# Optimization experiments

Hardware: AMD Instinct MI355X
Metric: run time of the kernel (lower is better)

## Reference

```python
import jax, jax.numpy as jnp
import numpy as np
from jax import lax


def _conv(x, W):
    # NCHW conv, stride 1, SAME padding (padding = kernel//2 in original)
    return lax.conv_general_dilated(x, W, (1, 1), 'SAME',
                                    dimension_numbers=('NCHW', 'OIHW', 'NCHW'))


def _cconv(zr, zi, Wr, Wi, br, bi):
    # complex conv: (zr + i*zi) * (Wr + i*Wi)
    yr = _conv(zr, Wr) - _conv(zi, Wi) + br[None, :, None, None]
    yi = _conv(zr, Wi) + _conv(zi, Wr) + bi[None, :, None, None]
    return yr, yi


def setup_inputs() -> dict:
    key = jax.random.key(0)
    B, C, H, W = 16, 128, 64, 64        # C = 128 total = 64 real + 64 imag channels
    half = C // 2                        # 64 complex channels
    kin = (C + C) // 2                   # (input+hidden)/2 complex input channels = 128
    K = 3
    ks = jax.random.split(key, 20)
    inp = {
        'x':      jax.random.normal(ks[0], (B, C, H, W), jnp.float32),
        'h_prev': jax.random.normal(ks[1], (B, C, H, W), jnp.float32),
        'c_prev': jax.random.normal(ks[2], (B, C, H, W), jnp.float32),
    }
    i = 3
    for g in ('i', 'f', 'o', 'c'):
        inp['Wr_' + g] = jax.random.normal(ks[i], (half, kin, K, K), jnp.float32) * 0.05; i += 1
        inp['Wi_' + g] = jax.random.normal(ks[i], (half, kin, K, K), jnp.float32) * 0.05; i += 1
        inp['br_' + g] = jax.random.normal(ks[i], (half,), jnp.float32) * 0.05; i += 1
        inp['bi_' + g] = jax.random.normal(ks[i], (half,), jnp.float32) * 0.05; i += 1
    return inp


def reference(x, h_prev, c_prev,
              Wr_i, Wi_i, br_i, bi_i,
              Wr_f, Wi_f, br_f, bi_f,
              Wr_o, Wi_o, br_o, bi_o,
              Wr_c, Wi_c, br_c, bi_c):
    C = x.shape[1]
    h = C // 2
    xr, xi = x[:, :h], x[:, h:]
    hr, hi = h_prev[:, :h], h_prev[:, h:]
    cr, ci = c_prev[:, :h], c_prev[:, h:]

    zr = jnp.concatenate([xr, hr], axis=1)   # real part of combined
    zi = jnp.concatenate([xi, hi], axis=1)   # imag part of combined

    # gates: complex conv then split sigmoid / tanh (applied per component)
    i_r, i_i = map(jax.nn.sigmoid, _cconv(zr, zi, Wr_i, Wi_i, br_i, bi_i))
    # f gate conv output is computed but unused in final update (original bug keeps x as f)
    o_r, o_i = map(jax.nn.sigmoid, _cconv(zr, zi, Wr_o, Wi_o, br_o, bi_o))
    ct_r, ct_i = map(jnp.tanh, _cconv(zr, zi, Wr_c, Wi_c, br_c, bi_c))

    # faithful to original: f_r/f_i taken from x, not from conv_f output
    c_new_r = xr * cr - xi * ci + i_r * ct_r - i_i * ct_i
    c_new_i = xr * ci + xi * cr + i_r * ct_i + i_i * ct_r

    t_r = jnp.tanh(c_new_r)
    t_i = jnp.tanh(c_new_i)
    h_new = jnp.concatenate([o_r * t_r - o_i * t_i, o_r * t_i + o_i * t_r], axis=1)
    c_new = jnp.concatenate([c_new_r, c_new_i], axis=1)
    return h_new, c_new
```

## Files before the change

kernel.cpp:

```cpp
#include <hip/hip_runtime.h>
#include <hip/hip_bf16.h>


typedef __attribute__((ext_vector_type(8))) short short8;
typedef __attribute__((ext_vector_type(4))) float floatx4;
typedef __attribute__((ext_vector_type(4))) float float4v;

#define HSIZE  8388608

__device__ __forceinline__ short f2bf(float f) {
  __hip_bfloat16 h = __float2bfloat16(f);
  return *reinterpret_cast<short*>(&h);
}

__device__ __forceinline__ float bf2f(short s) {
  unsigned u = ((unsigned)(unsigned short)s) << 16;
  return __uint_as_float(u);
}

__device__ __forceinline__ void gload16(const short* g, void* lds) {
  __builtin_amdgcn_global_load_lds(
      (__attribute__((address_space(1))) void*)(g),
      (__attribute__((address_space(3))) void*)(lds), 16, 0, 0);
}

__global__ __launch_bounds__(256) void prep_kernel(
    const float* __restrict__ xs, const float* __restrict__ hs,
    short* __restrict__ Zp,
    const float* __restrict__ Wr_i, const float* __restrict__ Wi_i,
    const float* __restrict__ Wr_o, const float* __restrict__ Wi_o,
    const float* __restrict__ Wr_c, const float* __restrict__ Wi_c,
    const float* __restrict__ br_i, const float* __restrict__ bi_i,
    const float* __restrict__ br_o, const float* __restrict__ bi_o,
    const float* __restrict__ br_c, const float* __restrict__ bi_c,
    short* __restrict__ Wp, float* __restrict__ bias) {
  __shared__ short tile[64 * 72];
  int blk = blockIdx.x;
  int tid = threadIdx.x;

  if (blk < 520) {
    int t = blk * 256 + tid;
    int s   = t & 31;
    int pix = t >> 5;
    int b = pix / 260;
    int r = pix - b * 260;
    int yp, xp;
    if (r < 66)       { yp = 0;               xp = r; }
    else if (r < 132) { yp = 65;              xp = r - 66; }
    else { int r2 = r - 132; yp = 1 + (r2 >> 1); xp = (r2 & 1) * 65; }
    short8 z;
#pragma unroll
    for (int q = 0; q < 8; ++q) z[q] = 0;
    *(short8*)(Zp + (((b * 66 + yp) * 66 + xp) * 256 + s * 8)) = z;
    return;
  }

  if (blk < 520 + 4096) {
    int bid = blk - 520;
    int y      = bid & 63;
    int half   = (bid >> 6) & 1;
    int srcSel = (bid >> 7) & 1;
    int b      = bid >> 8;
    const float* src = srcSel ? hs : xs;
    int chBase  = half * 64;
    int cinBase = half * 128 + srcSel * 64;
    int x4 = tid & 15, chq = tid >> 4;
#pragma unroll
    for (int p = 0; p < 4; ++p) {
      int ch = p * 16 + chq;
      float4v f = *(const float4v*)(src + (size_t)(b * 128 + chBase + ch) * 4096 + y * 64 + x4 * 4);
#pragma unroll
      for (int e = 0; e < 4; ++e)
        tile[(x4 * 4 + e) * 72 + ch] = f2bf(f[e]);
    }
    __syncthreads();
    int x = tid >> 2, seg = tid & 3;
    short8 v0 = *(const short8*)(tile + x * 72 + seg * 16);
    short8 v1 = *(const short8*)(tile + x * 72 + seg * 16 + 8);
    size_t outp = ((size_t)(b * 66 + y + 1) * 66 + x + 1) * 256 + cinBase + seg * 16;
    *(short8*)(Zp + outp)     = v0;
    *(short8*)(Zp + outp + 8) = v1;
    return;
  }

  {
    int g = (blk - 4616) * 256 + tid;
    if (g >= 384 * 9 * 256) return;
    int cin = g & 255;
    int tap = (g >> 8) % 9;
    int n   = g / (256 * 9);
    int part = n >> 6, ch = n & 63;
    const float *Wr, *Wi;
    if (part < 2)      { Wr = Wr_i; Wi = Wi_i; }
    else if (part < 4) { Wr = Wr_o; Wi = Wi_o; }
    else               { Wr = Wr_c; Wi = Wi_c; }
    int im = part & 1;
    int ci = cin & 127;
    int second = cin >> 7;
    const float* src = im ? (second ? Wr : Wi) : (second ? Wi : Wr);
    float f = src[(ch * 128 + ci) * 9 + tap];
    if (!im && second) f = -f;
    Wp[(n * 9 + tap) * 256 + cin] = f2bf(f);
    if (g < 384) {
      int p2 = g >> 6, c2 = g & 63;
      const float* bs = (p2 == 0) ? br_i : (p2 == 1) ? bi_i : (p2 == 2) ? br_o
                      : (p2 == 3) ? bi_o : (p2 == 4) ? br_c : bi_c;
      bias[g] = bs[c2];
    }
  }
}

__device__ __forceinline__ void issueA(const short* __restrict__ Wp, int tapkc,
                                       short8* dst, int tid, int wv) {
#pragma unroll
  for (int it = 0; it < 3; ++it) {
    int idx = tid + it * 512;
    int row = idx >> 2, p = idx & 3;
    int g = p ^ (row & 3);
    gload16(Wp + ((size_t)row * 2304 + tapkc + g * 8),
            (void*)(dst + (it * 512 + wv * 64)));
  }
}

__device__ __forceinline__ void issueBc(const short* __restrict__ Z, int zrow0,
                                        int kcn32, int tapc, short8* dst,
                                        int tid, int wv) {
  int idx = tapc * 512 + tid;
  int row = idx >> 8;
  int rem = idx & 255;
  int col = 1 + (rem >> 2);
  int p   = idx & 3;
  int g   = p ^ (col & 3);
  int base = tapc * 512 + wv * 64;
  int rowu = base >> 8;
  gload16(Z + ((size_t)((zrow0 + row) * 66 + col) * 256 + kcn32 + g * 8),
          (void*)(dst + (base + rowu * 8 + 4)));
}

template<int DYN, int DXN>
__device__ __forceinline__ void readFrags(const short8* __restrict__ Ab,
                                          const short8* __restrict__ Bb0,
                                          short8 (&af)[6], short8 (&bf)[4],
                                          int aBase, int wpx, int l15, int l4) {
  const short8* Bb = Bb0 + (wpx + DYN) * 264;
  int bb = (l15 + DXN) * 4 + (l4 ^ ((l15 + DXN) & 3));
#pragma unroll
  for (int i = 0; i < 6; ++i) af[i] = Ab[aBase + i * 64];
#pragma unroll
  for (int j = 0; j < 4; ++j) bf[j] = Bb[bb + j * 64];
}

__device__ __forceinline__ void mfma24(const short8 (&af)[6], const short8 (&bf)[4],
                                       floatx4 (&acc)[6][4]) {
  __builtin_amdgcn_s_setprio(1);
#pragma unroll
  for (int i = 0; i < 6; ++i)
#pragma unroll
    for (int j = 0; j < 4; ++j)
      acc[i][j] = __builtin_amdgcn_mfma_f32_16x16x32_bf16(af[i], bf[j], acc[i][j], 0, 0, 0);
  __builtin_amdgcn_s_setprio(0);
}

__device__ __forceinline__ float fsig(float v) { return 1.f / (1.f + __expf(-v)); }
__device__ __forceinline__ float ftanh(float v) {
  float e = __expf(2.f * v);
  return 1.f - 2.f / (e + 1.f);
}

__global__ __launch_bounds__(512, 2) void conv_fused(
    const short* __restrict__ Z, const short* __restrict__ Wp,
    const float* __restrict__ bias, const float* __restrict__ x,
    const float* __restrict__ c_prev, float* __restrict__ out) {
  __shared__ short8 As[2][1536];
  __shared__ short8 Bs[2][1056];

  const int tid = threadIdx.x;
  const int wv = tid >> 6, lane = tid & 63;
  const int l15 = lane & 15, l4 = lane >> 4;
  const int wc4 = wv & 3;
  const int wpx = wv >> 2;
  const int pb = blockIdx.x;
  const int b  = pb >> 5;
  const int y0 = (pb & 31) * 2;
  const int zrow0 = b * 66 + y0;

  const int aBase = (wc4 * 96 + l15) * 4 + (l4 ^ (l15 & 3));

  floatx4 acc[6][4];
#pragma unroll
  for (int i = 0; i < 6; ++i)
#pragma unroll
    for (int j = 0; j < 4; ++j)
#pragma unroll
      for (int r = 0; r < 4; ++r) acc[i][j][r] = 0.f;

  short8 afA[6], bfA[4], afB[6], bfB[4];

  if (tid < 64) {
    int buf = tid >> 5, w = tid & 31;
    int r = w >> 3, hi = (w >> 2) & 1, p = w & 3;
    short8 z;
#pragma unroll
    for (int q = 0; q < 8; ++q) z[q] = 0;
    Bs[buf][r * 264 + (hi ? 260 : 0) + p] = z;
  }
  issueA(Wp, 0, &As[0][0], tid, wv);
  issueBc(Z, zrow0, 0, 0, &Bs[0][0], tid, wv);
  issueBc(Z, zrow0, 0, 1, &Bs[0][0], tid, wv);
  issueA(Wp, 256, &As[1][0], tid, wv);
  __builtin_amdgcn_sched_barrier(0);
  asm volatile("s_waitcnt vmcnt(3) lgkmcnt(0)" ::: "memory");
  __builtin_amdgcn_sched_barrier(0);
  __builtin_amdgcn_s_barrier();
  __builtin_amdgcn_sched_barrier(0);
  readFrags<0, 0>(&As[0][0], &Bs[0][0], afA, bfA, aBase, wpx, l15, l4);

#define STEP(TAP, PE, KCV)                                                     \
  {                                                                            \
    constexpr int PS   = ((TAP) + (PE)) & 1;                                   \
    constexpr int TAPN = ((TAP) + 1) % 9;                                      \
    constexpr int PBN  = ((TAP) == 8) ? ((PE) ^ 1) : (PE);                     \
    if constexpr ((TAP) == 1 || (TAP) == 2)                                    \
      asm volatile("s_waitcnt vmcnt(1) lgkmcnt(0)" ::: "memory");              \
    else                                                                       \
      asm volatile("s_waitcnt vmcnt(0) lgkmcnt(0)" ::: "memory");              \
    __builtin_amdgcn_sched_barrier(0);                                         \
    __builtin_amdgcn_s_barrier();                                              \
    __builtin_amdgcn_sched_barrier(0);                                         \
    if constexpr (PS == 0)                                                     \
      readFrags<TAPN / 3, TAPN % 3>(&As[1][0], &Bs[PBN][0], afB, bfB,          \
                                    aBase, wpx, l15, l4);                      \
    else                                                                       \
      readFrags<TAPN / 3, TAPN % 3>(&As[0][0], &Bs[PBN][0], afA, bfA,          \
                                    aBase, wpx, l15, l4);                      \
    { const int kc2 = ((TAP) <= 6) ? (KCV) : (KCV) + 1;                        \
      issueA(Wp, (((TAP) + 2) % 9) * 256 + kc2 * 32, &As[PS][0], tid, wv); }   \
    if constexpr ((TAP) == 0 || (TAP) == 1)                                    \
      issueBc(Z, zrow0, ((KCV) + 1) * 32, (TAP), &Bs[(PE) ^ 1][0], tid, wv);   \
    if constexpr (PS == 0) mfma24(afA, bfA, acc);                              \
    else                   mfma24(afB, bfB, acc);                              \
  }

  for (int kq = 0; kq < 4; ++kq) {
    const int kE = kq * 2, kO = kE + 1;
    STEP(0, 0, kE) STEP(1, 0, kE) STEP(2, 0, kE) STEP(3, 0, kE) STEP(4, 0, kE)
    STEP(5, 0, kE) STEP(6, 0, kE) STEP(7, 0, kE) STEP(8, 0, kE)
    STEP(0, 1, kO) STEP(1, 1, kO) STEP(2, 1, kO) STEP(3, 1, kO) STEP(4, 1, kO)
    STEP(5, 1, kO) STEP(6, 1, kO) STEP(7, 1, kO) STEP(8, 1, kO)
  }
#undef STEP

  asm volatile("s_waitcnt vmcnt(0) lgkmcnt(0)" ::: "memory");
  __syncthreads();
  short* Ex = (short*)&As[0][0];
#pragma unroll
  for (int l = 0; l < 2; ++l) {
    if (wpx == l) {
#pragma unroll
      for (int i = 0; i < 6; ++i)
#pragma unroll
        for (int j = 0; j < 4; ++j)
#pragma unroll
          for (int rr = 0; rr < 4; ++rr) {
            int ch = wc4 * 96 + i * 16 + l4 * 4 + rr;
            int xx = j * 16 + l15;
            Ex[ch * 64 + xx] = f2bf(acc[i][j][rr] + bias[ch]);
          }
    }
    __syncthreads();
    {
      int xg = tid & 63, cg = tid >> 6;
#pragma unroll
      for (int k = 0; k < 8; ++k) {
        int c = cg * 8 + k;
        float yri = bf2f(Ex[(0 * 64 + c) * 64 + xg]);
        float yii = bf2f(Ex[(1 * 64 + c) * 64 + xg]);
        float yro = bf2f(Ex[(2 * 64 + c) * 64 + xg]);
        float yio = bf2f(Ex[(3 * 64 + c) * 64 + xg]);
        float yrc = bf2f(Ex[(4 * 64 + c) * 64 + xg]);
        float yic = bf2f(Ex[(5 * 64 + c) * 64 + xg]);
        float i_r = fsig(yri), i_i = fsig(yii);
        float o_r = fsig(yro), o_i = fsig(yio);
        float ct_r = ftanh(yrc), ct_i = ftanh(yic);
        int base = (b * 128 + c) * 4096 + (y0 + l) * 64 + xg;
        float xr = x[base];
        float xi = x[base + 64 * 4096];
        float cr = c_prev[base];
        float ci = c_prev[base + 64 * 4096];
        float cnr = xr * cr - xi * ci + i_r * ct_r - i_i * ct_i;
        float cni = xr * ci + xi * cr + i_r * ct_i + i_i * ct_r;
        float tr = ftanh(cnr), ti = ftanh(cni);
        out[base]                     = o_r * tr - o_i * ti;
        out[base + 64 * 4096]         = o_r * ti + o_i * tr;
        out[HSIZE + base]             = cnr;
        out[HSIZE + base + 64 * 4096] = cni;
      }
    }
    __syncthreads();
  }
}

extern "C" void kernel_launch(void* const* d_in, const int* in_sizes, int n_in,
                              void* d_out, int out_size, void* d_ws, size_t ws_size,
                              hipStream_t stream) {
  char* ws = (char*)d_ws;
  short* Zp   = (short*)ws;
  short* Wp   = (short*)(ws + 35684352);
  float* bias = (float*)(ws + 37453824);

  prep_kernel<<<8072, 256, 0, stream>>>(
      (const float*)d_in[0], (const float*)d_in[1], Zp,
      (const float*)d_in[3], (const float*)d_in[4],
      (const float*)d_in[11], (const float*)d_in[12],
      (const float*)d_in[15], (const float*)d_in[16],
      (const float*)d_in[5], (const float*)d_in[6],
      (const float*)d_in[13], (const float*)d_in[14],
      (const float*)d_in[17], (const float*)d_in[18],
      Wp, bias);
  conv_fused<<<512, 512, 0, stream>>>(
      Zp, Wp, bias, (const float*)d_in[0], (const float*)d_in[2],
      (float*)d_out);
}
```

Baseline: 310.0 us.

## Rework LDS swizzles for A/B tiles, drop prep transpose tile, pad epilogue staging

Changes the global-to-LDS load mapping for weight and input tiles so each row pair shares an 8-slot swizzled group, and updates the fragment reads to match, aiming to cut LDS bank conflicts in the MFMA loop. The prep kernel's activation transpose now builds bf16 channel vectors directly in registers from float2 loads, with no shared-memory tile or barrier. The epilogue staging buffer is split into two channel halves with a padded row stride of 68, which lowers bank conflicts but adds an extra barrier round per output row.

New measurement: 314.8 us. No clear change (+1.6%).

```diff
diff --git a/kernel.cpp b/kernel.cpp
--- a/kernel.cpp
+++ b/kernel.cpp
@@ -5,6 +5,7 @@
 typedef __attribute__((ext_vector_type(8))) short short8;
 typedef __attribute__((ext_vector_type(4))) float floatx4;
 typedef __attribute__((ext_vector_type(4))) float float4v;
+typedef __attribute__((ext_vector_type(2))) float float2v;
 
 #define HSIZE  8388608
 
@@ -34,7 +35,6 @@
     const float* __restrict__ br_o, const float* __restrict__ bi_o,
     const float* __restrict__ br_c, const float* __restrict__ bi_c,
     short* __restrict__ Wp, float* __restrict__ bias) {
-  __shared__ short tile[64 * 72];
   int blk = blockIdx.x;
   int tid = threadIdx.x;
 
@@ -64,22 +64,19 @@
     const float* src = srcSel ? hs : xs;
     int chBase  = half * 64;
     int cinBase = half * 128 + srcSel * 64;
-    int x4 = tid & 15, chq = tid >> 4;
-#pragma unroll
-    for (int p = 0; p < 4; ++p) {
-      int ch = p * 16 + chq;
-      float4v f = *(const float4v*)(src + (size_t)(b * 128 + chBase + ch) * 4096 + y * 64 + x4 * 4);
-#pragma unroll
-      for (int e = 0; e < 4; ++e)
-        tile[(x4 * 4 + e) * 72 + ch] = f2bf(f[e]);
+    int seg8 = tid & 7, xg = tid >> 3;
+    int x0 = xg * 2;
+    short8 v0, v1;
+#pragma unroll
+    for (int k = 0; k < 8; ++k) {
+      float2v f = *(const float2v*)(src +
+          (size_t)(b * 128 + chBase + seg8 * 8 + k) * 4096 + y * 64 + x0);
+      v0[k] = f2bf(f[0]);
+      v1[k] = f2bf(f[1]);
     }
-    __syncthreads();
-    int x = tid >> 2, seg = tid & 3;
-    short8 v0 = *(const short8*)(tile + x * 72 + seg * 16);
-    short8 v1 = *(const short8*)(tile + x * 72 + seg * 16 + 8);
-    size_t outp = ((size_t)(b * 66 + y + 1) * 66 + x + 1) * 256 + cinBase + seg * 16;
-    *(short8*)(Zp + outp)     = v0;
-    *(short8*)(Zp + outp + 8) = v1;
+    size_t outp = ((size_t)(b * 66 + y + 1) * 66 + x0 + 1) * 256 + cinBase + seg8 * 8;
+    *(short8*)(Zp + outp)       = v0;
+    *(short8*)(Zp + outp + 256) = v1;
     return;
   }
 
@@ -115,9 +112,11 @@
 #pragma unroll
   for (int it = 0; it < 3; ++it) {
     int idx = tid + it * 512;
-    int row = idx >> 2, p = idx & 3;
-    int g = p ^ (row & 3);
-    gload16(Wp + ((size_t)row * 2304 + tapkc + g * 8),
+    int rp  = idx >> 3;
+    int q   = idx & 7;
+    int row = rp * 2 + (q & 1);
+    int kg  = ((q >> 1) - rp) & 3;
+    gload16(Wp + ((size_t)row * 2304 + tapkc + kg * 8),
             (void*)(dst + (it * 512 + wv * 64)));
   }
 }
@@ -125,29 +124,35 @@
 __device__ __forceinline__ void issueBc(const short* __restrict__ Z, int zrow0,
                                         int kcn32, int tapc, short8* dst,
                                         int tid, int wv) {
-  int idx = tapc * 512 + tid;
-  int row = idx >> 8;
-  int rem = idx & 255;
-  int col = 1 + (rem >> 2);
-  int p   = idx & 3;
-  int g   = p ^ (col & 3);
-  int base = tapc * 512 + wv * 64;
-  int rowu = base >> 8;
-  gload16(Z + ((size_t)((zrow0 + row) * 66 + col) * 256 + kcn32 + g * 8),
-          (void*)(dst + (base + rowu * 8 + 4)));
+  int s   = tapc * 512 + tid;
+  int r   = s >> 8;
+  int off = s & 255;
+  int cp  = off >> 3;
+  int q   = off & 7;
+  int col = 1 + cp * 2 + (q & 1);
+  int kg  = ((q >> 1) - cp) & 3;
+  int s0  = tapc * 512 + wv * 64;
+  gload16(Z + ((size_t)((zrow0 + r) * 66 + col) * 256 + kcn32 + kg * 8),
+          (void*)(dst + ((s0 >> 8) * 264 + (s0 & 255))));
 }
 
 template<int DYN, int DXN>
 __device__ __forceinline__ void readFrags(const short8* __restrict__ Ab,
                                           const short8* __restrict__ Bb0,
                                           short8 (&af)[6], short8 (&bf)[4],
-                                          int aBase, int wpx, int l15, int l4) {
+                                          int aSlot, int wpx, int l15, int l4) {
   const short8* Bb = Bb0 + (wpx + DYN) * 264;
-  int bb = (l15 + DXN) * 4 + (l4 ^ ((l15 + DXN) & 3));
-#pragma unroll
-  for (int i = 0; i < 6; ++i) af[i] = Ab[aBase + i * 64];
-#pragma unroll
-  for (int j = 0; j < 4; ++j) bf[j] = Bb[bb + j * 64];
+#pragma unroll
+  for (int i = 0; i < 6; ++i) af[i] = Ab[aSlot + i * 64];
+#pragma unroll
+  for (int j = 0; j < 4; ++j) {
+    int col = j * 16 + l15 + DXN;
+    int cm  = col - 1;
+    int s   = (cm >> 1) * 8 + ((2 * l4 + (cm & 7)) & 7);
+    if (DXN == 0 && j == 0) { if (col == 0)  s = 256 + l4; }
+    if (DXN == 2 && j == 3) { if (col == 65) s = 260 + l4; }
+    bf[j] = Bb[s];
+  }
 }
 
 __device__ __forceinline__ void mfma24(const short8 (&af)[6], const short8 (&bf)[4],
@@ -184,7 +189,7 @@
   const int y0 = (pb & 31) * 2;
   const int zrow0 = b * 66 + y0;
 
-  const int aBase = (wc4 * 96 + l15) * 4 + (l4 ^ (l15 & 3));
+  const int aSlot = (wc4 * 48 + (l15 >> 1)) * 8 + ((2 * l4 + (l15 & 7)) & 7);
 
   floatx4 acc[6][4];
 #pragma unroll
@@ -197,12 +202,12 @@
   short8 afA[6], bfA[4], afB[6], bfB[4];
 
   if (tid < 64) {
-    int buf = tid >> 5, w = tid & 31;
-    int r = w >> 3, hi = (w >> 2) & 1, p = w & 3;
+    int buf = tid >> 5, w5 = tid & 31;
+    int r = w5 >> 3, h = (w5 >> 2) & 1, kg = w5 & 3;
     short8 z;
 #pragma unroll
     for (int q = 0; q < 8; ++q) z[q] = 0;
-    Bs[buf][r * 264 + (hi ? 260 : 0) + p] = z;
+    Bs[buf][r * 264 + 256 + h * 4 + kg] = z;
   }
   issueA(Wp, 0, &As[0][0], tid, wv);
   issueBc(Z, zrow0, 0, 0, &Bs[0][0], tid, wv);
@@ -213,7 +218,7 @@
   __builtin_amdgcn_sched_barrier(0);
   __builtin_amdgcn_s_barrier();
   __builtin_amdgcn_sched_barrier(0);
-  readFrags<0, 0>(&As[0][0], &Bs[0][0], afA, bfA, aBase, wpx, l15, l4);
+  readFrags<0, 0>(&As[0][0], &Bs[0][0], afA, bfA, aSlot, wpx, l15, l4);
 
 #define STEP(TAP, PE, KCV)                                                     \
   {                                                                            \
@@ -229,10 +234,10 @@
     __builtin_amdgcn_sched_barrier(0);                                         \
     if constexpr (PS == 0)                                                     \
       readFrags<TAPN / 3, TAPN % 3>(&As[1][0], &Bs[PBN][0], afB, bfB,          \
-                                    aBase, wpx, l15, l4);                      \
+                                    aSlot, wpx, l15, l4);                      \
     else                                                                       \
       readFrags<TAPN / 3, TAPN % 3>(&As[0][0], &Bs[PBN][0], afA, bfA,          \
-                                    aBase, wpx, l15, l4);                      \
+                                    aSlot, wpx, l15, l4);                      \
     { const int kc2 = ((TAP) <= 6) ? (KCV) : (KCV) + 1;                        \
       issueA(Wp, (((TAP) + 2) % 9) * 256 + kc2 * 32, &As[PS][0], tid, wv); }   \
     if constexpr ((TAP) == 0 || (TAP) == 1)                                    \
@@ -255,48 +260,56 @@
   short* Ex = (short*)&As[0][0];
 #pragma unroll
   for (int l = 0; l < 2; ++l) {
-    if (wpx == l) {
-#pragma unroll
-      for (int i = 0; i < 6; ++i)
-#pragma unroll
-        for (int j = 0; j < 4; ++j)
-#pragma unroll
-          for (int rr = 0; rr < 4; ++rr) {
-            int ch = wc4 * 96 + i * 16 + l4 * 4 + rr;
-            int xx = j * 16 + l15;
-            Ex[ch * 64 + xx] = f2bf(acc[i][j][rr] + bias[ch]);
+#pragma unroll
+    for (int hf = 0; hf < 2; ++hf) {
+      if (wpx == l) {
+#pragma unroll
+        for (int i = 0; i < 6; ++i) {
+          int chb = wc4 * 96 + i * 16;
+          if (((chb >> 5) & 1) == hf) {
+#pragma unroll
+            for (int j = 0; j < 4; ++j)
+#pragma unroll
+              for (int rr = 0; rr < 4; ++rr) {
+                int ch = chb + l4 * 4 + rr;
+                int row = (ch >> 6) * 32 + (ch & 31);
+                Ex[row * 68 + j * 16 + l15] = f2bf(acc[i][j][rr] + bias[ch]);
+              }
           }
+        }
+      }
+      __syncthreads();
+      {
+        int xg = tid & 63, cg = tid >> 6;
+#pragma unroll
+        for (int k = 0; k < 4; ++k) {
+          int c5 = cg * 4 + k;
+          int c  = hf * 32 + c5;
+          float yri = bf2f(Ex[(0 * 32 + c5) * 68 + xg]);
+          float yii = bf2f(Ex[(1 * 32 + c5) * 68 + xg]);
+          float yro = bf2f(Ex[(2 * 32 + c5) * 68 + xg]);
+          float yio = bf2f(Ex[(3 * 32 + c5) * 68 + xg]);
+          float yrc = bf2f(Ex[(4 * 32 + c5) * 68 + xg]);
+          float yic = bf2f(Ex[(5 * 32 + c5) * 68 + xg]);
+          float i_r = fsig(yri), i_i = fsig(yii);
+          float o_r = fsig(yro), o_i = fsig(yio);
+          float ct_r = ftanh(yrc), ct_i = ftanh(yic);
+          int base = (b * 128 + c) * 4096 + (y0 + l) * 64 + xg;
+          float xr = x[base];
+          float xi = x[base + 64 * 4096];
+          float cr = c_prev[base];
+          float ci = c_prev[base + 64 * 4096];
+          float cnr = xr * cr - xi * ci + i_r * ct_r - i_i * ct_i;
+          float cni = xr * ci + xi * cr + i_r * ct_i + i_i * ct_r;
+          float tr = ftanh(cnr), ti = ftanh(cni);
+          out[base]                     = o_r * tr - o_i * ti;
+          out[base + 64 * 4096]         = o_r * ti + o_i * tr;
+          out[HSIZE + base]             = cnr;
+          out[HSIZE + base + 64 * 4096] = cni;
+        }
+      }
+      __syncthreads();
     }
-    __syncthreads();
-    {
-      int xg = tid & 63, cg = tid >> 6;
-#pragma unroll
-      for (int k = 0; k < 8; ++k) {
-        int c = cg * 8 + k;
-        float yri = bf2f(Ex[(0 * 64 + c) * 64 + xg]);
-        float yii = bf2f(Ex[(1 * 64 + c) * 64 + xg]);
-        float yro = bf2f(Ex[(2 * 64 + c) * 64 + xg]);
-        float yio = bf2f(Ex[(3 * 64 + c) * 64 + xg]);
-        float yrc = bf2f(Ex[(4 * 64 + c) * 64 + xg]);
-        float yic = bf2f(Ex[(5 * 64 + c) * 64 + xg]);
-        float i_r = fsig(yri), i_i = fsig(yii);
-        float o_r = fsig(yro), o_i = fsig(yio);
-        float ct_r = ftanh(yrc), ct_i = ftanh(yic);
-        int base = (b * 128 + c) * 4096 + (y0 + l) * 64 + xg;
-        float xr = x[base];
-        float xi = x[base + 64 * 4096];
-        float cr = c_prev[base];
-        float ci = c_prev[base + 64 * 4096];
-        float cnr = xr * cr - xi * ci + i_r * ct_r - i_i * ct_i;
-        float cni = xr * ci + xi * cr + i_r * ct_i + i_i * ct_r;
-        float tr = ftanh(cnr), ti = ftanh(cni);
-        out[base]                     = o_r * tr - o_i * ti;
-        out[base + 64 * 4096]         = o_r * ti + o_i * tr;
-        out[HSIZE + base]             = cnr;
-        out[HSIZE + base + 64 * 4096] = cni;
-      }
-    }
-    __syncthreads();
   }
 }
 
```
